# Kernel tuning notes

Hardware: AMD Instinct MI355X
Metric: run time of the kernel (lower is better)

The kernel has to match this reference:

```python
import jax, jax.numpy as jnp
import numpy as np

SHIFT = 1  # torch module picks +/-1 randomly at init; fixed to +1 for determinism


def setup_inputs() -> dict:
    key = jax.random.key(0)
    k1, k2 = jax.random.split(key)
    x = jax.random.normal(k1, (1, 512, 14, 14), dtype=jnp.float32)
    w = jax.random.normal(k2, (256, 256, 3), dtype=jnp.float32)
    return {"x": x, "w": w}


def reference(x, w):
    # (1,512,14,14) -> (1, o=2, i=256, H=14, W=14)
    t = x.reshape(1, 2, 256, 14, 14)
    # roll along W by +1 (torch.roll dim 4)
    t = jnp.roll(t, SHIFT, axis=4)
    # unfold(kernel=(3,1), padding=(1,0)) over the W axis after the
    # (1,7168,14,1) collapse == zero-padded 3-tap sliding windows along W.
    p = jnp.pad(t, ((0, 0), (0, 0), (0, 0), (0, 0), (1, 1)))
    # taps: (1,2,256,14,3,14) == (l,o,i,n,j,m) of the torch reshape
    taps = jnp.stack([p[..., 0:14], p[..., 1:15], p[..., 2:16]], axis=4)
    # 3-tap conv1d along W: contract input channel i and tap j
    out = jnp.einsum('loinjm,ikj->loknm', taps, w)  # (1,2,256,14,14)
    out = out.reshape(1, 512, 14, 14)
    # final roll along H (torch dim 2 of (1,512,14,14))
    out = jnp.roll(out, SHIFT, axis=2)
    return out
```

## Files before the change

kernel.cpp:

```cpp
#include <hip/hip_runtime.h>


#define BLOCK_THREADS 448

__global__ __launch_bounds__(BLOCK_THREADS) void shiftconv_kernel(
    const float* __restrict__ x,
    const float* __restrict__ w,
    float* __restrict__ out)
{
    __shared__ float xs[256 * 16];

    const int kt = blockIdx.x;
    const int h  = blockIdx.y;
    const int o  = blockIdx.z;
    const int t  = threadIdx.x;
    const int n  = (h + 13) % 14;

    for (int e = t; e < 512; e += BLOCK_THREADS) {
        int i = e >> 1;
        xs[i * 16 + (e & 1) * 15] = 0.0f;
    }
    for (int e = t; e < 256 * 14; e += BLOCK_THREADS) {
        int i  = e / 14;
        int ww = e - i * 14;
        float v = x[((size_t)(o * 256 + i) * 14 + n) * 14 + ww];
        int q = (ww <= 12) ? (ww + 2) : 1;
        xs[i * 16 + q] = v;
    }
    __syncthreads();

    const int kk = t & 31;
    const int m  = t >> 5;
    const int kglob = kt * 32 + kk;

    const float* wp = w + (size_t)kglob * 3;
    const float* xp = xs + m;

    float acc = 0.0f;
#pragma unroll 8
    for (int i = 0; i < 256; ++i) {
        float w0 = wp[0];
        float w1 = wp[1];
        float w2 = wp[2];
        acc = fmaf(xp[0], w0, acc);
        acc = fmaf(xp[1], w1, acc);
        acc = fmaf(xp[2], w2, acc);
        wp += 768;
        xp += 16;
    }

    out[((size_t)(o * 256 + kglob) * 14 + h) * 14 + m] = acc;
}

extern "C" void kernel_launch(void* const* d_in, const int* in_sizes, int n_in,
                              void* d_out, int out_size, void* d_ws, size_t ws_size,
                              hipStream_t stream) {
    const float* x = (const float*)d_in[0];
    const float* w = (const float*)d_in[1];
    float* out = (float*)d_out;

    dim3 grid(8, 14, 2);
    dim3 block(BLOCK_THREADS);
    shiftconv_kernel<<<grid, block, 0, stream>>>(x, w, out);
}
```

Measured before the change: 70.05 us.

## Split input-channel reduction four ways and compute two outputs per thread

Doubles the block to 896 threads and splits the 256-channel reduction into four 64-channel slices, combining partial sums through shared memory. Each thread now computes two adjacent output columns, reusing the three weight taps and overlapping input values, and loads them with vector float3/float2 loads. Two independent accumulators per output shorten the FMA dependency chain. The cost is an extra shared buffer, a second barrier and a serial reduction step.

After: 63.35 us. 9.6% less time.

```diff
diff --git a/kernel.cpp b/kernel.cpp
--- a/kernel.cpp
+++ b/kernel.cpp
@@ -1,14 +1,15 @@
 #include <hip/hip_runtime.h>
 
 
-#define BLOCK_THREADS 448
+#define BT 896
 
-__global__ __launch_bounds__(BLOCK_THREADS) void shiftconv_kernel(
+__global__ __launch_bounds__(BT) void shiftconv_kernel(
     const float* __restrict__ x,
     const float* __restrict__ w,
     float* __restrict__ out)
 {
     __shared__ float xs[256 * 16];
+    __shared__ float part[3 * 7 * 64];
 
     const int kt = blockIdx.x;
     const int h  = blockIdx.y;
@@ -16,40 +17,56 @@
     const int t  = threadIdx.x;
     const int n  = (h + 13) % 14;
 
-    for (int e = t; e < 512; e += BLOCK_THREADS) {
-        int i = e >> 1;
-        xs[i * 16 + (e & 1) * 15] = 0.0f;
-    }
-    for (int e = t; e < 256 * 14; e += BLOCK_THREADS) {
+    for (int e = t; e < 512; e += BT)
+        xs[(e >> 1) * 16 + (e & 1) * 15] = 0.0f;
+    for (int e = t; e < 256 * 14; e += BT) {
         int i  = e / 14;
         int ww = e - i * 14;
         float v = x[((size_t)(o * 256 + i) * 14 + n) * 14 + ww];
-        int q = (ww <= 12) ? (ww + 2) : 1;
-        xs[i * 16 + q] = v;
+        xs[i * 16 + ((ww <= 12) ? (ww + 2) : 1)] = v;
     }
     __syncthreads();
 
     const int kk = t & 31;
-    const int m  = t >> 5;
+    const int s  = (t >> 5) & 3;
+    const int mp = t >> 7;
     const int kglob = kt * 32 + kk;
+    const int m0 = 2 * mp;
 
-    const float* wp = w + (size_t)kglob * 3;
-    const float* xp = xs + m;
+    const float* wp = w + ((size_t)(s * 64) * 256 + kglob) * 3;
+    const float* xp = xs + (s * 64) * 16 + m0;
 
-    float acc = 0.0f;
-#pragma unroll 8
-    for (int i = 0; i < 256; ++i) {
-        float w0 = wp[0];
-        float w1 = wp[1];
-        float w2 = wp[2];
-        acc = fmaf(xp[0], w0, acc);
-        acc = fmaf(xp[1], w1, acc);
-        acc = fmaf(xp[2], w2, acc);
+    float a0 = 0.f, a1 = 0.f, b0 = 0.f, b1 = 0.f;
+#pragma unroll 4
+    for (int i = 0; i < 64; ++i) {
+        float3 wv  = *reinterpret_cast<const float3*>(wp);
+        float2 t01 = *reinterpret_cast<const float2*>(xp);
+        float2 t23 = *reinterpret_cast<const float2*>(xp + 2);
+        a0 = fmaf(t01.x, wv.x, a0);
+        a1 = fmaf(t01.y, wv.y, a1);
+        a0 = fmaf(t23.x, wv.z, a0);
+        b0 = fmaf(t01.y, wv.x, b0);
+        b1 = fmaf(t23.x, wv.y, b1);
+        b0 = fmaf(t23.y, wv.z, b0);
         wp += 768;
         xp += 16;
     }
+    float am = a0 + a1, bm = b0 + b1;
 
-    out[((size_t)(o * 256 + kglob) * 14 + h) * 14 + m] = acc;
+    if (s) {
+        int base = ((s - 1) * 7 + mp) * 64 + kk * 2;
+        part[base]     = am;
+        part[base + 1] = bm;
+    }
+    __syncthreads();
+    if (s == 0) {
+        int base = mp * 64 + kk * 2;
+        am += part[base]     + part[448 + base]     + part[896 + base];
+        bm += part[base + 1] + part[448 + base + 1] + part[896 + base + 1];
+        size_t off = ((size_t)(o * 256 + kglob) * 14 + h) * 14 + m0;
+        out[off]     = am;
+        out[off + 1] = bm;
+    }
 }
 
 extern "C" void kernel_launch(void* const* d_in, const int* in_sizes, int n_in,
@@ -60,6 +77,6 @@
     float* out = (float*)d_out;
 
     dim3 grid(8, 14, 2);
-    dim3 block(BLOCK_THREADS);
+    dim3 block(BT);
     shiftconv_kernel<<<grid, block, 0, stream>>>(x, w, out);
 }
```

## Split input-channel reduction across threads with register-tiled outputs and smem reduce

Applied to the files above, without the earlier changes.

Each thread now handles 2 output channels by all 14 output positions over an 8-channel slice of the input, instead of one output over all 256 input channels. Shared-memory rows are read with float4 loads, which gives register reuse of x and w, and the serial 256-step dependent FMA chain becomes short independent chains. Partial sums from the 32 channel slices are written to shared memory, reused from the input buffer, and reduced by 448 threads. The cost is more registers, two extra barriers and a 32-way shared-memory reduction.

After: 60.06 us. 1.17x faster.

```diff
diff --git a/kernel.cpp b/kernel.cpp
--- a/kernel.cpp
+++ b/kernel.cpp
@@ -1,14 +1,16 @@
 #include <hip/hip_runtime.h>
 
 
-#define BLOCK_THREADS 448
+#define BT 512
 
-__global__ __launch_bounds__(BLOCK_THREADS) void shiftconv_kernel(
+__global__ __launch_bounds__(BT) void shiftconv_kernel(
     const float* __restrict__ x,
     const float* __restrict__ w,
     float* __restrict__ out)
 {
-    __shared__ float xs[256 * 16];
+    __shared__ __align__(16) float smem[32 * 28 * 17 + 2];
+    float* xs   = smem;
+    float* part = smem;
 
     const int kt = blockIdx.x;
     const int h  = blockIdx.y;
@@ -16,40 +18,70 @@
     const int t  = threadIdx.x;
     const int n  = (h + 13) % 14;
 
-    for (int e = t; e < 512; e += BLOCK_THREADS) {
-        int i = e >> 1;
-        xs[i * 16 + (e & 1) * 15] = 0.0f;
-    }
-    for (int e = t; e < 256 * 14; e += BLOCK_THREADS) {
+    xs[(t >> 1) * 16 + (t & 1) * 15] = 0.0f;
+    for (int e = t; e < 256 * 14; e += BT) {
         int i  = e / 14;
         int ww = e - i * 14;
         float v = x[((size_t)(o * 256 + i) * 14 + n) * 14 + ww];
-        int q = (ww <= 12) ? (ww + 2) : 1;
-        xs[i * 16 + q] = v;
+        xs[i * 16 + ((ww <= 12) ? (ww + 2) : 1)] = v;
     }
     __syncthreads();
 
-    const int kk = t & 31;
-    const int m  = t >> 5;
-    const int kglob = kt * 32 + kk;
+    const int kk2 = t & 15;
+    const int s   = t >> 4;
+    const int kg0 = kt * 32 + 2 * kk2;
+    const int i0  = s * 8;
 
-    const float* wp = w + (size_t)kglob * 3;
-    const float* xp = xs + m;
+    const float* wp = w + ((size_t)i0 * 256 + kg0) * 3;
+    const float* xp = xs + i0 * 16;
 
-    float acc = 0.0f;
-#pragma unroll 8
-    for (int i = 0; i < 256; ++i) {
-        float w0 = wp[0];
-        float w1 = wp[1];
-        float w2 = wp[2];
-        acc = fmaf(xp[0], w0, acc);
-        acc = fmaf(xp[1], w1, acc);
-        acc = fmaf(xp[2], w2, acc);
+    float accA[14], accB[14];
+#pragma unroll
+    for (int m = 0; m < 14; ++m) { accA[m] = 0.f; accB[m] = 0.f; }
+
+#pragma unroll
+    for (int i = 0; i < 8; ++i) {
+        float4 q0 = *reinterpret_cast<const float4*>(xp);
+        float4 q1 = *reinterpret_cast<const float4*>(xp + 4);
+        float4 q2 = *reinterpret_cast<const float4*>(xp + 8);
+        float4 q3 = *reinterpret_cast<const float4*>(xp + 12);
+        float r[16] = {q0.x,q0.y,q0.z,q0.w, q1.x,q1.y,q1.z,q1.w,
+                       q2.x,q2.y,q2.z,q2.w, q3.x,q3.y,q3.z,q3.w};
+        float3 wa = *reinterpret_cast<const float3*>(wp);
+        float3 wb = *reinterpret_cast<const float3*>(wp + 3);
+#pragma unroll
+        for (int m = 0; m < 14; ++m) {
+            accA[m] = fmaf(r[m],   wa.x, accA[m]);
+            accA[m] = fmaf(r[m+1], wa.y, accA[m]);
+            accA[m] = fmaf(r[m+2], wa.z, accA[m]);
+            accB[m] = fmaf(r[m],   wb.x, accB[m]);
+            accB[m] = fmaf(r[m+1], wb.y, accB[m]);
+            accB[m] = fmaf(r[m+2], wb.z, accB[m]);
+        }
+        xp += 16;
         wp += 768;
-        xp += 16;
     }
 
-    out[((size_t)(o * 256 + kglob) * 14 + h) * 14 + m] = acc;
+    __syncthreads();
+
+#pragma unroll
+    for (int m = 0; m < 14; ++m) {
+        part[(s * 28 + m)      * 17 + kk2] = accA[m];
+        part[(s * 28 + 14 + m) * 17 + kk2] = accB[m];
+    }
+    __syncthreads();
+
+    if (t < 448) {
+        int kk = t & 31;
+        int m  = t >> 5;
+        int k2 = kk >> 1;
+        int mu = (kk & 1) * 14 + m;
+        float sum = 0.f;
+#pragma unroll
+        for (int si = 0; si < 32; ++si)
+            sum += part[(si * 28 + mu) * 17 + k2];
+        out[((size_t)(o * 256 + kt * 32 + kk) * 14 + h) * 14 + m] = sum;
+    }
 }
 
 extern "C" void kernel_launch(void* const* d_in, const int* in_sizes, int n_in,
@@ -60,6 +92,6 @@
     float* out = (float*)d_out;
 
     dim3 grid(8, 14, 2);
-    dim3 block(BLOCK_THREADS);
+    dim3 block(BT);
     shiftconv_kernel<<<grid, block, 0, stream>>>(x, w, out);
 }
```
